# Kernel tuning notes

Hardware: AMD Instinct MI355X
Metric: run time of the kernel (lower is better)

The kernel has to match this reference:

```python
import jax, jax.numpy as jnp
import numpy as np

FEATURE = 256
HIDDEN = 256

def setup_inputs() -> dict:
    key = jax.random.key(0)
    k1, k2, k3 = jax.random.split(key, 3)
    x = jax.random.normal(k1, (64, 2048, FEATURE), dtype=jnp.float32)
    # xavier_normal with gain=0.1: std = 0.1 * sqrt(2/(fan_in+fan_out))
    std_x = 0.1 * np.sqrt(2.0 / (FEATURE + 4 * HIDDEN))
    std_h = 0.1 * np.sqrt(2.0 / (HIDDEN + 4 * HIDDEN))
    WeightX = jax.random.normal(k2, (FEATURE, 4 * HIDDEN), dtype=jnp.float32) * std_x
    WeightH = jax.random.normal(k3, (HIDDEN, 4 * HIDDEN), dtype=jnp.float32) * std_h
    BiasX = jnp.zeros((4 * HIDDEN,), dtype=jnp.float32)
    BiasH = jnp.zeros((4 * HIDDEN,), dtype=jnp.float32)
    return {"x": x, "WeightX": WeightX, "WeightH": WeightH, "BiasX": BiasX, "BiasH": BiasH}

def reference(x, WeightX, WeightH, BiasX, BiasH):
    bs, T, _ = x.shape
    H = WeightH.shape[0]
    # precompute input projection for all timesteps: (bs, T, 4H)
    x_proj = jnp.einsum('btf,fg->btg', x, WeightX) + BiasX + BiasH

    def step(carry, xp_t):
        h, c = carry
        gates = xp_t + h @ WeightH  # (bs, 4H)
        i = jax.nn.sigmoid(gates[:, :H])
        f = jax.nn.sigmoid(gates[:, H:2 * H])
        g = jnp.tanh(gates[:, 2 * H:3 * H])
        o = jax.nn.sigmoid(gates[:, 3 * H:])
        c = f * c + i * g
        h = o * jnp.tanh(c)
        return (h, c), h

    h0 = jnp.zeros((bs, H), dtype=x.dtype)
    c0 = jnp.zeros((bs, H), dtype=x.dtype)
    (h_n, _), out_t = jax.lax.scan(step, (h0, c0), jnp.swapaxes(x_proj, 0, 1))
    output = jnp.swapaxes(out_t, 0, 1)  # (bs, T, H)
    return output, h_n
```

## Files before the change

### kernel.cpp

```cpp
#include <hip/hip_runtime.h>
#include <hip/hip_fp16.h>

#define BATCH 64
#define TSEQ  2048
#define FEAT  256
#define HID   256
#define G4    1024

typedef _Float16 half2_t __attribute__((ext_vector_type(2)));

__device__ __forceinline__ float dot2acc_u(unsigned int a, unsigned int b, float acc) {
    half2_t ah = __builtin_bit_cast(half2_t, a);
    half2_t bh = __builtin_bit_cast(half2_t, b);
#if __has_builtin(__builtin_amdgcn_fdot2)
    return __builtin_amdgcn_fdot2(ah, bh, acc, false);
#else
    return acc + (float)ah.x * (float)bh.x + (float)ah.y * (float)bh.y;
#endif
}

__device__ __forceinline__ float sig_f(float x)  { return 1.f / (1.f + __expf(-x)); }
__device__ __forceinline__ float tanh_f(float x) { return 1.f - 2.f / (__expf(2.f * x) + 1.f); }

__device__ __forceinline__ unsigned int pack2(float a, float b) {
    half2_t h = { (_Float16)a, (_Float16)b };
    return __builtin_bit_cast(unsigned int, h);
}

template <int CTRL>
__device__ __forceinline__ float dpp_add(float x) {
    int y = __builtin_amdgcn_update_dpp(0, __builtin_bit_cast(int, x), CTRL, 0xf, 0xf, true);
    return x + __builtin_bit_cast(float, y);
}

__global__ void wt_convert(const float* __restrict__ WH, uint4* __restrict__ WS,
                           uint4* __restrict__ WST) {
    int idx = blockIdx.x * 256 + threadIdx.x;
    int u = idx >> 13;
    int r = idx & 8191;
    int p = r >> 9;
    int tid = r & 511;
    int w = tid >> 6, c = (tid >> 3) & 7, s = tid & 7;
    int j = p * 64 + w * 8 + c;
    int k0 = 32 * s + 8 * u;
    uint4 v;
    v.x = pack2(WH[(k0 + 0) * G4 + j], WH[(k0 + 1) * G4 + j]);
    v.y = pack2(WH[(k0 + 2) * G4 + j], WH[(k0 + 3) * G4 + j]);
    v.z = pack2(WH[(k0 + 4) * G4 + j], WH[(k0 + 5) * G4 + j]);
    v.w = pack2(WH[(k0 + 6) * G4 + j], WH[(k0 + 7) * G4 + j]);
    if (p < 13) {
        WS[u * 8192 + p * 512 + tid] = v;
    } else {
        int q = p - 13;
        WST[(q * 4 + u) * 512 + tid] = v;
        WST[6144 + (q * 4 + u) * 512 + tid] = v;
    }
}

__global__ __launch_bounds__(256) void xproj_gemm(
    const float* __restrict__ X, const float* __restrict__ WX,
    const float* __restrict__ BX, const float* __restrict__ BH,
    _Float16* __restrict__ XP)
{
    __shared__ float As[64][17];
    __shared__ float Bs[16][68];

    const int tid = threadIdx.x;
    const int tx = tid & 15;
    const int ty = tid >> 4;
    const int rowBase = blockIdx.y * 64;
    const int colBase = blockIdx.x * 64;

    const int ea = tid * 4;
    const int ar = ea >> 4, ac = ea & 15;
    const int br = ea >> 6, bc = ea & 63;

    float acc[4][4] = {};

    for (int kt = 0; kt < FEAT; kt += 16) {
        float4 av = *(const float4*)(X  + (size_t)(rowBase + ar) * FEAT + kt + ac);
        float4 bv = *(const float4*)(WX + (size_t)(kt + br) * G4 + colBase + bc);
        As[ar][ac + 0] = av.x; As[ar][ac + 1] = av.y;
        As[ar][ac + 2] = av.z; As[ar][ac + 3] = av.w;
        *(float4*)&Bs[br][bc] = bv;
        __syncthreads();
        #pragma unroll
        for (int kk = 0; kk < 16; ++kk) {
            float4 b = *(const float4*)&Bs[kk][tx * 4];
            float a0 = As[ty * 4 + 0][kk];
            float a1 = As[ty * 4 + 1][kk];
            float a2 = As[ty * 4 + 2][kk];
            float a3 = As[ty * 4 + 3][kk];
            acc[0][0] = fmaf(a0, b.x, acc[0][0]); acc[0][1] = fmaf(a0, b.y, acc[0][1]);
            acc[0][2] = fmaf(a0, b.z, acc[0][2]); acc[0][3] = fmaf(a0, b.w, acc[0][3]);
            acc[1][0] = fmaf(a1, b.x, acc[1][0]); acc[1][1] = fmaf(a1, b.y, acc[1][1]);
            acc[1][2] = fmaf(a1, b.z, acc[1][2]); acc[1][3] = fmaf(a1, b.w, acc[1][3]);
            acc[2][0] = fmaf(a2, b.x, acc[2][0]); acc[2][1] = fmaf(a2, b.y, acc[2][1]);
            acc[2][2] = fmaf(a2, b.z, acc[2][2]); acc[2][3] = fmaf(a2, b.w, acc[2][3]);
            acc[3][0] = fmaf(a3, b.x, acc[3][0]); acc[3][1] = fmaf(a3, b.y, acc[3][1]);
            acc[3][2] = fmaf(a3, b.z, acc[3][2]); acc[3][3] = fmaf(a3, b.w, acc[3][3]);
        }
        __syncthreads();
    }

    const int n0 = colBase + tx * 4;
    float4 bxv = *(const float4*)(BX + n0);
    float4 bhv = *(const float4*)(BH + n0);
    float bb0 = bxv.x + bhv.x, bb1 = bxv.y + bhv.y;
    float bb2 = bxv.z + bhv.z, bb3 = bxv.w + bhv.w;

    #pragma unroll
    for (int i = 0; i < 4; ++i) {
        int row = rowBase + ty * 4 + i;
        _Float16* p = XP + (size_t)row * G4 + n0;
        half2_t p01 = { (_Float16)(acc[i][0] + bb0), (_Float16)(acc[i][1] + bb1) };
        half2_t p23 = { (_Float16)(acc[i][2] + bb2), (_Float16)(acc[i][3] + bb3) };
        *(half2_t*)(p + 0) = p01;
        *(half2_t*)(p + 2) = p23;
    }
}

#define DO_PASS(P, W0, W1, W2, W3)                                              \
    {                                                                           \
        float acc = 0.f;                                                        \
        acc = dot2acc_u(hr0.x, (W0).x, acc); acc = dot2acc_u(hr0.y, (W0).y, acc); \
        acc = dot2acc_u(hr0.z, (W0).z, acc); acc = dot2acc_u(hr0.w, (W0).w, acc); \
        acc = dot2acc_u(hr1.x, (W1).x, acc); acc = dot2acc_u(hr1.y, (W1).y, acc); \
        acc = dot2acc_u(hr1.z, (W1).z, acc); acc = dot2acc_u(hr1.w, (W1).w, acc); \
        acc = dot2acc_u(hr2.x, (W2).x, acc); acc = dot2acc_u(hr2.y, (W2).y, acc); \
        acc = dot2acc_u(hr2.z, (W2).z, acc); acc = dot2acc_u(hr2.w, (W2).w, acc); \
        acc = dot2acc_u(hr3.x, (W3).x, acc); acc = dot2acc_u(hr3.y, (W3).y, acc); \
        acc = dot2acc_u(hr3.z, (W3).z, acc); acc = dot2acc_u(hr3.w, (W3).w, acc); \
        acc = dpp_add<0xB1>(acc);                                               \
        acc = dpp_add<0x4E>(acc);                                               \
        acc = dpp_add<0x141>(acc);                                              \
        if (s == 0) g_sh[(P) * 64 + w * 8 + c] = acc;                           \
    }

__global__ __launch_bounds__(512, 2) void lstm_rec(
    const _Float16* __restrict__ XP, const uint4* __restrict__ WS,
    const uint4* __restrict__ WST, float* __restrict__ OUT)
{
    __shared__ uint4 LDS_W[4 * 512];
    __shared__ float g_sh[G4];
    __shared__ __align__(16) unsigned short hs[4][64];

    const int tid = threadIdx.x;
    const int b = blockIdx.x;
    const int w = tid >> 6;
    const int c = (tid >> 3) & 7;
    const int s = tid & 7;

    uint4 wreg[48];
    #pragma unroll
    for (int p = 0; p < 12; ++p) {
        #pragma unroll
        for (int u = 0; u < 4; ++u)
            wreg[p * 4 + u] = WS[u * 8192 + p * 512 + tid];
    }
    #pragma unroll
    for (int u = 0; u < 4; ++u)
        LDS_W[u * 512 + tid] = WS[u * 8192 + 12 * 512 + tid];

    if (tid < 256) ((unsigned short*)hs)[tid] = 0;
    float cst = 0.f, hlast = 0.f;
    const _Float16* xpb = XP + (size_t)b * TSEQ * G4;
    float* outb = OUT + (size_t)b * TSEQ * HID;
    __syncthreads();

    #pragma unroll 1
    for (int t = 0; t < TSEQ; ++t) {
        uint4 hr0 = ((const uint4*)(&hs[0][0]))[s];
        uint4 hr1 = ((const uint4*)(&hs[1][0]))[s];
        uint4 hr2 = ((const uint4*)(&hs[2][0]))[s];
        uint4 hr3 = ((const uint4*)(&hs[3][0]))[s];

        float xv0 = 0.f, xv1 = 0.f, xv2 = 0.f, xv3 = 0.f;
        if (tid < 256) {
            const _Float16* xq = xpb + (size_t)t * G4;
            xv0 = (float)xq[tid];       xv1 = (float)xq[tid + 256];
            xv2 = (float)xq[tid + 512]; xv3 = (float)xq[tid + 768];
        }

        const uint4* stb = WST + (size_t)(t & 1) * 6144;
        uint4 pf0 = stb[(0 * 4 + 0) * 512 + tid];
        uint4 pf1 = stb[(0 * 4 + 1) * 512 + tid];
        uint4 pf2 = stb[(0 * 4 + 2) * 512 + tid];
        uint4 pf3 = stb[(0 * 4 + 3) * 512 + tid];

        DO_PASS(0,  wreg[0],  wreg[1],  wreg[2],  wreg[3]);
        DO_PASS(1,  wreg[4],  wreg[5],  wreg[6],  wreg[7]);
        DO_PASS(2,  wreg[8],  wreg[9],  wreg[10], wreg[11]);
        DO_PASS(3,  wreg[12], wreg[13], wreg[14], wreg[15]);
        DO_PASS(4,  wreg[16], wreg[17], wreg[18], wreg[19]);
        DO_PASS(5,  wreg[20], wreg[21], wreg[22], wreg[23]);

        DO_PASS(13, pf0, pf1, pf2, pf3);
        pf0 = stb[(1 * 4 + 0) * 512 + tid];
        pf1 = stb[(1 * 4 + 1) * 512 + tid];
        pf2 = stb[(1 * 4 + 2) * 512 + tid];
        pf3 = stb[(1 * 4 + 3) * 512 + tid];

        DO_PASS(6,  wreg[24], wreg[25], wreg[26], wreg[27]);
        DO_PASS(7,  wreg[28], wreg[29], wreg[30], wreg[31]);
        DO_PASS(8,  wreg[32], wreg[33], wreg[34], wreg[35]);
        DO_PASS(9,  wreg[36], wreg[37], wreg[38], wreg[39]);
        DO_PASS(10, wreg[40], wreg[41], wreg[42], wreg[43]);
        DO_PASS(11, wreg[44], wreg[45], wreg[46], wreg[47]);

        DO_PASS(14, pf0, pf1, pf2, pf3);
        pf0 = stb[(2 * 4 + 0) * 512 + tid];
        pf1 = stb[(2 * 4 + 1) * 512 + tid];
        pf2 = stb[(2 * 4 + 2) * 512 + tid];
        pf3 = stb[(2 * 4 + 3) * 512 + tid];

        {
            uint4 l0 = LDS_W[0 * 512 + tid];
            uint4 l1 = LDS_W[1 * 512 + tid];
            uint4 l2 = LDS_W[2 * 512 + tid];
            uint4 l3 = LDS_W[3 * 512 + tid];
            DO_PASS(12, l0, l1, l2, l3);
        }
        DO_PASS(15, pf0, pf1, pf2, pf3);

        __syncthreads();

        if (tid < 256) {
            float gi = sig_f(g_sh[tid] + xv0);
            float gf = sig_f(g_sh[tid + 256] + xv1);
            float gg = tanh_f(g_sh[tid + 512] + xv2);
            float go = sig_f(g_sh[tid + 768] + xv3);
            cst = gf * cst + gi * gg;
            float h = go * tanh_f(cst);
            outb[(size_t)t * HID + tid] = h;
            hlast = h;
            hs[(tid >> 3) & 3][(tid >> 5) * 8 + (tid & 7)] =
                __builtin_bit_cast(unsigned short, (_Float16)h);
        }
        __syncthreads();
    }

    if (tid < 256)
        OUT[(size_t)BATCH * TSEQ * HID + (size_t)b * HID + tid] = hlast;
}

extern "C" void kernel_launch(void* const* d_in, const int* in_sizes, int n_in,
                              void* d_out, int out_size, void* d_ws, size_t ws_size,
                              hipStream_t stream) {
    const float* x  = (const float*)d_in[0];
    const float* wx = (const float*)d_in[1];
    const float* wh = (const float*)d_in[2];
    const float* bx = (const float*)d_in[3];
    const float* bh = (const float*)d_in[4];
    float* out = (float*)d_out;

    _Float16* xp = (_Float16*)d_ws;
    uint4* ws = (uint4*)((char*)d_ws + (size_t)BATCH * TSEQ * G4 * sizeof(_Float16));
    uint4* wst = ws + 32768;

    hipLaunchKernelGGL(wt_convert, dim3(128), dim3(256), 0, stream, wh, ws, wst);
    hipLaunchKernelGGL(xproj_gemm, dim3(G4 / 64, (BATCH * TSEQ) / 64), dim3(256), 0, stream,
                       x, wx, bx, bh, xp);
    hipLaunchKernelGGL(lstm_rec, dim3(BATCH), dim3(512), 0, stream, xp, ws, wst, out);
}
```

Baseline: 5.674 ms.

## Rebalance recurrent weight residency across registers, LDS and streamed global, prefetch next x-projection

Changes how the recurrent weight matrix is split. Nine gate passes now stay in registers (down from twelve), three sit in LDS (up from one), and four are streamed from global each step (up from three); the duplicated double-buffer copy of the streamed weights is dropped. The next timestep's x-projection load is issued in the middle of the current step so its latency is hidden, and each dot product uses two accumulators to shorten the dependency chain. The aim is to cut register pressure and spills and to overlap load latency on the serial recurrence, at the cost of more LDS and global traffic per step.

```diff
diff --git a/kernel.cpp b/kernel.cpp
--- a/kernel.cpp
+++ b/kernel.cpp
@@ -48,12 +48,11 @@
     v.y = pack2(WH[(k0 + 2) * G4 + j], WH[(k0 + 3) * G4 + j]);
     v.z = pack2(WH[(k0 + 4) * G4 + j], WH[(k0 + 5) * G4 + j]);
     v.w = pack2(WH[(k0 + 6) * G4 + j], WH[(k0 + 7) * G4 + j]);
-    if (p < 13) {
+    if (p < 12) {
         WS[u * 8192 + p * 512 + tid] = v;
     } else {
-        int q = p - 13;
+        int q = p - 12;
         WST[(q * 4 + u) * 512 + tid] = v;
-        WST[6144 + (q * 4 + u) * 512 + tid] = v;
     }
 }
 
@@ -122,26 +121,36 @@
 
 #define DO_PASS(P, W0, W1, W2, W3)                                              \
     {                                                                           \
-        float acc = 0.f;                                                        \
-        acc = dot2acc_u(hr0.x, (W0).x, acc); acc = dot2acc_u(hr0.y, (W0).y, acc); \
-        acc = dot2acc_u(hr0.z, (W0).z, acc); acc = dot2acc_u(hr0.w, (W0).w, acc); \
-        acc = dot2acc_u(hr1.x, (W1).x, acc); acc = dot2acc_u(hr1.y, (W1).y, acc); \
-        acc = dot2acc_u(hr1.z, (W1).z, acc); acc = dot2acc_u(hr1.w, (W1).w, acc); \
-        acc = dot2acc_u(hr2.x, (W2).x, acc); acc = dot2acc_u(hr2.y, (W2).y, acc); \
-        acc = dot2acc_u(hr2.z, (W2).z, acc); acc = dot2acc_u(hr2.w, (W2).w, acc); \
-        acc = dot2acc_u(hr3.x, (W3).x, acc); acc = dot2acc_u(hr3.y, (W3).y, acc); \
-        acc = dot2acc_u(hr3.z, (W3).z, acc); acc = dot2acc_u(hr3.w, (W3).w, acc); \
+        float a0_ = 0.f, a1_ = 0.f;                                             \
+        a0_ = dot2acc_u(hr0.x, (W0).x, a0_); a0_ = dot2acc_u(hr0.y, (W0).y, a0_); \
+        a0_ = dot2acc_u(hr0.z, (W0).z, a0_); a0_ = dot2acc_u(hr0.w, (W0).w, a0_); \
+        a1_ = dot2acc_u(hr1.x, (W1).x, a1_); a1_ = dot2acc_u(hr1.y, (W1).y, a1_); \
+        a1_ = dot2acc_u(hr1.z, (W1).z, a1_); a1_ = dot2acc_u(hr1.w, (W1).w, a1_); \
+        a0_ = dot2acc_u(hr2.x, (W2).x, a0_); a0_ = dot2acc_u(hr2.y, (W2).y, a0_); \
+        a0_ = dot2acc_u(hr2.z, (W2).z, a0_); a0_ = dot2acc_u(hr2.w, (W2).w, a0_); \
+        a1_ = dot2acc_u(hr3.x, (W3).x, a1_); a1_ = dot2acc_u(hr3.y, (W3).y, a1_); \
+        a1_ = dot2acc_u(hr3.z, (W3).z, a1_); a1_ = dot2acc_u(hr3.w, (W3).w, a1_); \
+        float acc = a0_ + a1_;                                                  \
         acc = dpp_add<0xB1>(acc);                                               \
         acc = dpp_add<0x4E>(acc);                                               \
         acc = dpp_add<0x141>(acc);                                              \
         if (s == 0) g_sh[(P) * 64 + w * 8 + c] = acc;                           \
     }
 
+#define LDS_PASS(PP)                                                            \
+    {                                                                           \
+        uint4 l0 = LDS_W[((PP) * 4 + 0) * 512 + tid];                           \
+        uint4 l1 = LDS_W[((PP) * 4 + 1) * 512 + tid];                           \
+        uint4 l2 = LDS_W[((PP) * 4 + 2) * 512 + tid];                           \
+        uint4 l3 = LDS_W[((PP) * 4 + 3) * 512 + tid];                           \
+        DO_PASS(9 + (PP), l0, l1, l2, l3);                                      \
+    }
+
 __global__ __launch_bounds__(512, 2) void lstm_rec(
     const _Float16* __restrict__ XP, const uint4* __restrict__ WS,
     const uint4* __restrict__ WST, float* __restrict__ OUT)
 {
-    __shared__ uint4 LDS_W[4 * 512];
+    __shared__ uint4 LDS_W[3 * 4 * 512];
     __shared__ float g_sh[G4];
     __shared__ __align__(16) unsigned short hs[4][64];
 
@@ -151,21 +160,35 @@
     const int c = (tid >> 3) & 7;
     const int s = tid & 7;
 
-    uint4 wreg[48];
-    #pragma unroll
-    for (int p = 0; p < 12; ++p) {
+    uint4 wreg[36];
+    #pragma unroll
+    for (int p = 0; p < 9; ++p) {
         #pragma unroll
         for (int u = 0; u < 4; ++u)
             wreg[p * 4 + u] = WS[u * 8192 + p * 512 + tid];
     }
     #pragma unroll
-    for (int u = 0; u < 4; ++u)
-        LDS_W[u * 512 + tid] = WS[u * 8192 + 12 * 512 + tid];
+    for (int i = 0; i < 36; ++i)
+        asm volatile("" : "+v"(wreg[i].x), "+v"(wreg[i].y),
+                          "+v"(wreg[i].z), "+v"(wreg[i].w));
+
+    #pragma unroll
+    for (int pp = 0; pp < 3; ++pp) {
+        #pragma unroll
+        for (int u = 0; u < 4; ++u)
+            LDS_W[(pp * 4 + u) * 512 + tid] = WS[u * 8192 + (9 + pp) * 512 + tid];
+    }
 
     if (tid < 256) ((unsigned short*)hs)[tid] = 0;
     float cst = 0.f, hlast = 0.f;
     const _Float16* xpb = XP + (size_t)b * TSEQ * G4;
     float* outb = OUT + (size_t)b * TSEQ * HID;
+
+    float xv0 = 0.f, xv1 = 0.f, xv2 = 0.f, xv3 = 0.f;
+    if (tid < 256) {
+        xv0 = (float)xpb[tid];       xv1 = (float)xpb[tid + 256];
+        xv2 = (float)xpb[tid + 512]; xv3 = (float)xpb[tid + 768];
+    }
     __syncthreads();
 
     #pragma unroll 1
@@ -175,52 +198,58 @@
         uint4 hr2 = ((const uint4*)(&hs[2][0]))[s];
         uint4 hr3 = ((const uint4*)(&hs[3][0]))[s];
 
-        float xv0 = 0.f, xv1 = 0.f, xv2 = 0.f, xv3 = 0.f;
-        if (tid < 256) {
-            const _Float16* xq = xpb + (size_t)t * G4;
-            xv0 = (float)xq[tid];       xv1 = (float)xq[tid + 256];
-            xv2 = (float)xq[tid + 512]; xv3 = (float)xq[tid + 768];
-        }
-
-        const uint4* stb = WST + (size_t)(t & 1) * 6144;
+        uintptr_t stb_i = (uintptr_t)WST;
+        asm volatile("" : "+s"(stb_i));
+        const uint4* stb = (const uint4*)stb_i;
+
         uint4 pf0 = stb[(0 * 4 + 0) * 512 + tid];
         uint4 pf1 = stb[(0 * 4 + 1) * 512 + tid];
         uint4 pf2 = stb[(0 * 4 + 2) * 512 + tid];
         uint4 pf3 = stb[(0 * 4 + 3) * 512 + tid];
 
-        DO_PASS(0,  wreg[0],  wreg[1],  wreg[2],  wreg[3]);
-        DO_PASS(1,  wreg[4],  wreg[5],  wreg[6],  wreg[7]);
-        DO_PASS(2,  wreg[8],  wreg[9],  wreg[10], wreg[11]);
-        DO_PASS(3,  wreg[12], wreg[13], wreg[14], wreg[15]);
-        DO_PASS(4,  wreg[16], wreg[17], wreg[18], wreg[19]);
-        DO_PASS(5,  wreg[20], wreg[21], wreg[22], wreg[23]);
-
-        DO_PASS(13, pf0, pf1, pf2, pf3);
+        DO_PASS(0, wreg[0],  wreg[1],  wreg[2],  wreg[3]);
+        DO_PASS(1, wreg[4],  wreg[5],  wreg[6],  wreg[7]);
+        DO_PASS(2, wreg[8],  wreg[9],  wreg[10], wreg[11]);
+        DO_PASS(3, wreg[12], wreg[13], wreg[14], wreg[15]);
+
+        DO_PASS(12, pf0, pf1, pf2, pf3);
         pf0 = stb[(1 * 4 + 0) * 512 + tid];
         pf1 = stb[(1 * 4 + 1) * 512 + tid];
         pf2 = stb[(1 * 4 + 2) * 512 + tid];
         pf3 = stb[(1 * 4 + 3) * 512 + tid];
 
-        DO_PASS(6,  wreg[24], wreg[25], wreg[26], wreg[27]);
-        DO_PASS(7,  wreg[28], wreg[29], wreg[30], wreg[31]);
-        DO_PASS(8,  wreg[32], wreg[33], wreg[34], wreg[35]);
-        DO_PASS(9,  wreg[36], wreg[37], wreg[38], wreg[39]);
-        DO_PASS(10, wreg[40], wreg[41], wreg[42], wreg[43]);
-        DO_PASS(11, wreg[44], wreg[45], wreg[46], wreg[47]);
-
-        DO_PASS(14, pf0, pf1, pf2, pf3);
+        DO_PASS(4, wreg[16], wreg[17], wreg[18], wreg[19]);
+        DO_PASS(5, wreg[20], wreg[21], wreg[22], wreg[23]);
+        DO_PASS(6, wreg[24], wreg[25], wreg[26], wreg[27]);
+
+        DO_PASS(13, pf0, pf1, pf2, pf3);
         pf0 = stb[(2 * 4 + 0) * 512 + tid];
         pf1 = stb[(2 * 4 + 1) * 512 + tid];
         pf2 = stb[(2 * 4 + 2) * 512 + tid];
         pf3 = stb[(2 * 4 + 3) * 512 + tid];
 
+        DO_PASS(7, wreg[28], wreg[29], wreg[30], wreg[31]);
+        DO_PASS(8, wreg[32], wreg[33], wreg[34], wreg[35]);
+        LDS_PASS(0);
+
+        DO_PASS(14, pf0, pf1, pf2, pf3);
+        pf0 = stb[(3 * 4 + 0) * 512 + tid];
+        pf1 = stb[(3 * 4 + 1) * 512 + tid];
+        pf2 = stb[(3 * 4 + 2) * 512 + tid];
+        pf3 = stb[(3 * 4 + 3) * 512 + tid];
+
+        float xn0 = 0.f, xn1 = 0.f, xn2 = 0.f, xn3 = 0.f;
         {
-            uint4 l0 = LDS_W[0 * 512 + tid];
-            uint4 l1 = LDS_W[1 * 512 + tid];
-            uint4 l2 = LDS_W[2 * 512 + tid];
-            uint4 l3 = LDS_W[3 * 512 + tid];
-            DO_PASS(12, l0, l1, l2, l3);
+            int tn = (t + 1 < TSEQ) ? (t + 1) : t;
+            if (tid < 256) {
+                const _Float16* xq = xpb + (size_t)tn * G4;
+                xn0 = (float)xq[tid];       xn1 = (float)xq[tid + 256];
+                xn2 = (float)xq[tid + 512]; xn3 = (float)xq[tid + 768];
+            }
         }
+
+        LDS_PASS(1);
+        LDS_PASS(2);
         DO_PASS(15, pf0, pf1, pf2, pf3);
 
         __syncthreads();
@@ -237,6 +266,7 @@
             hs[(tid >> 3) & 3][(tid >> 5) * 8 + (tid & 7)] =
                 __builtin_bit_cast(unsigned short, (_Float16)h);
         }
+        xv0 = xn0; xv1 = xn1; xv2 = xn2; xv3 = xn3;
         __syncthreads();
     }
 
```

New measurement: 6.410 ms. +13.0%, slower.

## Split each batch's LSTM recurrence across two blocks with global h exchange

Applied to the files above, without the earlier changes.

Each batch row is now handled by a pair of workgroups, each owning half of the hidden units, so the recurrent weights fit entirely in LDS plus AGPRs and no weights are streamed from global memory each step. The partner's half of h is exchanged every timestep through global memory using release/acquire sequence counters and spin-waiting. The local-half dot products are computed before waiting, to overlap with the exchange, and the next step's input projection is prefetched one step ahead. The cost is a cross-workgroup synchronisation on every timestep, which relies on both blocks of a pair being resident at the same time and adds latency on the serial critical path.

```diff
diff --git a/kernel.cpp b/kernel.cpp
--- a/kernel.cpp
+++ b/kernel.cpp
@@ -34,27 +34,24 @@
 }
 
 __global__ void wt_convert(const float* __restrict__ WH, uint4* __restrict__ WS,
-                           uint4* __restrict__ WST) {
+                           unsigned* __restrict__ SEQ) {
+    if (blockIdx.x == 0 && threadIdx.x < 128) SEQ[threadIdx.x * 32] = 0;
     int idx = blockIdx.x * 256 + threadIdx.x;
-    int u = idx >> 13;
-    int r = idx & 8191;
-    int p = r >> 9;
-    int tid = r & 511;
+    int tid = idx & 511;
+    int u = (idx >> 9) & 3;
+    int pass = (idx >> 11) & 7;
+    int parity = (idx >> 14) & 1;
     int w = tid >> 6, c = (tid >> 3) & 7, s = tid & 7;
-    int j = p * 64 + w * 8 + c;
-    int k0 = 32 * s + 8 * u;
+    int jl = pass * 64 + w * 8 + c;
+    int j = (jl >> 7) * 256 + parity * 128 + (jl & 127);
+    int half_base = ((u < 2) ? parity : 1 - parity) * 128;
+    int k0 = half_base + 16 * s + 8 * (u & 1);
     uint4 v;
     v.x = pack2(WH[(k0 + 0) * G4 + j], WH[(k0 + 1) * G4 + j]);
     v.y = pack2(WH[(k0 + 2) * G4 + j], WH[(k0 + 3) * G4 + j]);
     v.z = pack2(WH[(k0 + 4) * G4 + j], WH[(k0 + 5) * G4 + j]);
     v.w = pack2(WH[(k0 + 6) * G4 + j], WH[(k0 + 7) * G4 + j]);
-    if (p < 13) {
-        WS[u * 8192 + p * 512 + tid] = v;
-    } else {
-        int q = p - 13;
-        WST[(q * 4 + u) * 512 + tid] = v;
-        WST[6144 + (q * 4 + u) * 512 + tid] = v;
-    }
+    WS[((parity * 8 + pass) * 4 + u) * 512 + tid] = v;
 }
 
 __global__ __launch_bounds__(256) void xproj_gemm(
@@ -120,128 +117,192 @@
     }
 }
 
-#define DO_PASS(P, W0, W1, W2, W3)                                              \
+#define DOT8(ACC, H0, H1, W0, W1)                                               \
+    ACC = dot2acc_u((H0).x, (W0).x, ACC); ACC = dot2acc_u((H0).y, (W0).y, ACC); \
+    ACC = dot2acc_u((H0).z, (W0).z, ACC); ACC = dot2acc_u((H0).w, (W0).w, ACC); \
+    ACC = dot2acc_u((H1).x, (W1).x, ACC); ACC = dot2acc_u((H1).y, (W1).y, ACC); \
+    ACC = dot2acc_u((H1).z, (W1).z, ACC); ACC = dot2acc_u((H1).w, (W1).w, ACC);
+
+#define AG_RD(d, a_) asm("v_accvgpr_read_b32 %0, %1" : "=v"(d) : "a"(a_), "s"(t))
+
+#define AG_DOT8(ACC, H0, H1, I0, I1)                                            \
     {                                                                           \
-        float acc = 0.f;                                                        \
-        acc = dot2acc_u(hr0.x, (W0).x, acc); acc = dot2acc_u(hr0.y, (W0).y, acc); \
-        acc = dot2acc_u(hr0.z, (W0).z, acc); acc = dot2acc_u(hr0.w, (W0).w, acc); \
-        acc = dot2acc_u(hr1.x, (W1).x, acc); acc = dot2acc_u(hr1.y, (W1).y, acc); \
-        acc = dot2acc_u(hr1.z, (W1).z, acc); acc = dot2acc_u(hr1.w, (W1).w, acc); \
-        acc = dot2acc_u(hr2.x, (W2).x, acc); acc = dot2acc_u(hr2.y, (W2).y, acc); \
-        acc = dot2acc_u(hr2.z, (W2).z, acc); acc = dot2acc_u(hr2.w, (W2).w, acc); \
-        acc = dot2acc_u(hr3.x, (W3).x, acc); acc = dot2acc_u(hr3.y, (W3).y, acc); \
-        acc = dot2acc_u(hr3.z, (W3).z, acc); acc = dot2acc_u(hr3.w, (W3).w, acc); \
-        acc = dpp_add<0xB1>(acc);                                               \
-        acc = dpp_add<0x4E>(acc);                                               \
-        acc = dpp_add<0x141>(acc);                                              \
-        if (s == 0) g_sh[(P) * 64 + w * 8 + c] = acc;                           \
+        unsigned q0, q1, q2, q3, q4, q5, q6, q7;                                \
+        AG_RD(q0, wa[I0].x); AG_RD(q1, wa[I0].y);                               \
+        AG_RD(q2, wa[I0].z); AG_RD(q3, wa[I0].w);                               \
+        AG_RD(q4, wa[I1].x); AG_RD(q5, wa[I1].y);                               \
+        AG_RD(q6, wa[I1].z); AG_RD(q7, wa[I1].w);                               \
+        ACC = dot2acc_u((H0).x, q0, ACC); ACC = dot2acc_u((H0).y, q1, ACC);     \
+        ACC = dot2acc_u((H0).z, q2, ACC); ACC = dot2acc_u((H0).w, q3, ACC);     \
+        ACC = dot2acc_u((H1).x, q4, ACC); ACC = dot2acc_u((H1).y, q5, ACC);     \
+        ACC = dot2acc_u((H1).z, q6, ACC); ACC = dot2acc_u((H1).w, q7, ACC);     \
     }
 
 __global__ __launch_bounds__(512, 2) void lstm_rec(
     const _Float16* __restrict__ XP, const uint4* __restrict__ WS,
-    const uint4* __restrict__ WST, float* __restrict__ OUT)
+    unsigned* __restrict__ EXD, unsigned* __restrict__ SEQ,
+    float* __restrict__ OUT)
 {
-    __shared__ uint4 LDS_W[4 * 512];
-    __shared__ float g_sh[G4];
-    __shared__ __align__(16) unsigned short hs[4][64];
+    __shared__ uint4 LDS_W[4 * 4 * 512];
+    __shared__ float g_sh[512];
+    __shared__ __align__(16) unsigned short hs[256];
 
     const int tid = threadIdx.x;
-    const int b = blockIdx.x;
+    const int parity = blockIdx.x & 1;
+    const int pair = blockIdx.x >> 1;
     const int w = tid >> 6;
     const int c = (tid >> 3) & 7;
     const int s = tid & 7;
 
-    uint4 wreg[48];
+    unsigned* seq_self = SEQ + (pair * 2 + parity) * 32;
+    unsigned* seq_par  = SEQ + (pair * 2 + (1 - parity)) * 32;
+    unsigned* exd_self = EXD + (pair * 2 + parity) * 2 * 64;
+    unsigned* exd_par  = EXD + (pair * 2 + (1 - parity)) * 2 * 64;
+
+    uint4 wa[16];
     #pragma unroll
-    for (int p = 0; p < 12; ++p) {
+    for (int p = 0; p < 4; ++p) {
+        #pragma unroll
+        for (int u = 0; u < 4; ++u) {
+            uint4 v = WS[((parity * 8 + (4 + p)) * 4 + u) * 512 + tid];
+            asm("v_accvgpr_write_b32 %0, %1" : "=a"(wa[p * 4 + u].x) : "v"(v.x));
+            asm("v_accvgpr_write_b32 %0, %1" : "=a"(wa[p * 4 + u].y) : "v"(v.y));
+            asm("v_accvgpr_write_b32 %0, %1" : "=a"(wa[p * 4 + u].z) : "v"(v.z));
+            asm("v_accvgpr_write_b32 %0, %1" : "=a"(wa[p * 4 + u].w) : "v"(v.w));
+        }
+    }
+    #pragma unroll
+    for (int p = 0; p < 4; ++p) {
         #pragma unroll
         for (int u = 0; u < 4; ++u)
-            wreg[p * 4 + u] = WS[u * 8192 + p * 512 + tid];
-    }
-    #pragma unroll
-    for (int u = 0; u < 4; ++u)
-        LDS_W[u * 512 + tid] = WS[u * 8192 + 12 * 512 + tid];
-
-    if (tid < 256) ((unsigned short*)hs)[tid] = 0;
-    float cst = 0.f, hlast = 0.f;
-    const _Float16* xpb = XP + (size_t)b * TSEQ * G4;
-    float* outb = OUT + (size_t)b * TSEQ * HID;
+            LDS_W[(p * 4 + u) * 512 + tid] = WS[((parity * 8 + p) * 4 + u) * 512 + tid];
+    }
+
+    if (tid < 128) ((unsigned*)hs)[tid] = 0;
+
+    const int pbase = parity * 128;
+    const _Float16* xpb = XP + (size_t)pair * TSEQ * G4;
+    float* outb = OUT + (size_t)pair * TSEQ * HID;
+
+    float c0 = 0.f, c1 = 0.f, hl0 = 0.f, hl1 = 0.f;
+    unsigned xv0 = 0, xv1 = 0, xv2 = 0, xv3 = 0;
+    if (tid < 64) {
+        const _Float16* xq = xpb;
+        xv0 = *(const unsigned*)(xq + 0 * 256 + pbase + 2 * tid);
+        xv1 = *(const unsigned*)(xq + 1 * 256 + pbase + 2 * tid);
+        xv2 = *(const unsigned*)(xq + 2 * 256 + pbase + 2 * tid);
+        xv3 = *(const unsigned*)(xq + 3 * 256 + pbase + 2 * tid);
+    }
     __syncthreads();
 
     #pragma unroll 1
     for (int t = 0; t < TSEQ; ++t) {
-        uint4 hr0 = ((const uint4*)(&hs[0][0]))[s];
-        uint4 hr1 = ((const uint4*)(&hs[1][0]))[s];
-        uint4 hr2 = ((const uint4*)(&hs[2][0]))[s];
-        uint4 hr3 = ((const uint4*)(&hs[3][0]))[s];
-
-        float xv0 = 0.f, xv1 = 0.f, xv2 = 0.f, xv3 = 0.f;
-        if (tid < 256) {
-            const _Float16* xq = xpb + (size_t)t * G4;
-            xv0 = (float)xq[tid];       xv1 = (float)xq[tid + 256];
-            xv2 = (float)xq[tid + 512]; xv3 = (float)xq[tid + 768];
-        }
-
-        const uint4* stb = WST + (size_t)(t & 1) * 6144;
-        uint4 pf0 = stb[(0 * 4 + 0) * 512 + tid];
-        uint4 pf1 = stb[(0 * 4 + 1) * 512 + tid];
-        uint4 pf2 = stb[(0 * 4 + 2) * 512 + tid];
-        uint4 pf3 = stb[(0 * 4 + 3) * 512 + tid];
-
-        DO_PASS(0,  wreg[0],  wreg[1],  wreg[2],  wreg[3]);
-        DO_PASS(1,  wreg[4],  wreg[5],  wreg[6],  wreg[7]);
-        DO_PASS(2,  wreg[8],  wreg[9],  wreg[10], wreg[11]);
-        DO_PASS(3,  wreg[12], wreg[13], wreg[14], wreg[15]);
-        DO_PASS(4,  wreg[16], wreg[17], wreg[18], wreg[19]);
-        DO_PASS(5,  wreg[20], wreg[21], wreg[22], wreg[23]);
-
-        DO_PASS(13, pf0, pf1, pf2, pf3);
-        pf0 = stb[(1 * 4 + 0) * 512 + tid];
-        pf1 = stb[(1 * 4 + 1) * 512 + tid];
-        pf2 = stb[(1 * 4 + 2) * 512 + tid];
-        pf3 = stb[(1 * 4 + 3) * 512 + tid];
-
-        DO_PASS(6,  wreg[24], wreg[25], wreg[26], wreg[27]);
-        DO_PASS(7,  wreg[28], wreg[29], wreg[30], wreg[31]);
-        DO_PASS(8,  wreg[32], wreg[33], wreg[34], wreg[35]);
-        DO_PASS(9,  wreg[36], wreg[37], wreg[38], wreg[39]);
-        DO_PASS(10, wreg[40], wreg[41], wreg[42], wreg[43]);
-        DO_PASS(11, wreg[44], wreg[45], wreg[46], wreg[47]);
-
-        DO_PASS(14, pf0, pf1, pf2, pf3);
-        pf0 = stb[(2 * 4 + 0) * 512 + tid];
-        pf1 = stb[(2 * 4 + 1) * 512 + tid];
-        pf2 = stb[(2 * 4 + 2) * 512 + tid];
-        pf3 = stb[(2 * 4 + 3) * 512 + tid];
-
-        {
-            uint4 l0 = LDS_W[0 * 512 + tid];
-            uint4 l1 = LDS_W[1 * 512 + tid];
-            uint4 l2 = LDS_W[2 * 512 + tid];
-            uint4 l3 = LDS_W[3 * 512 + tid];
-            DO_PASS(12, l0, l1, l2, l3);
-        }
-        DO_PASS(15, pf0, pf1, pf2, pf3);
-
-        __syncthreads();
-
-        if (tid < 256) {
-            float gi = sig_f(g_sh[tid] + xv0);
-            float gf = sig_f(g_sh[tid + 256] + xv1);
-            float gg = tanh_f(g_sh[tid + 512] + xv2);
-            float go = sig_f(g_sh[tid + 768] + xv3);
-            cst = gf * cst + gi * gg;
-            float h = go * tanh_f(cst);
-            outb[(size_t)t * HID + tid] = h;
-            hlast = h;
-            hs[(tid >> 3) & 3][(tid >> 5) * 8 + (tid & 7)] =
-                __builtin_bit_cast(unsigned short, (_Float16)h);
-        }
-        __syncthreads();
-    }
-
-    if (tid < 256)
-        OUT[(size_t)BATCH * TSEQ * HID + (size_t)b * HID + tid] = hlast;
+        const uint4* hso = (const uint4*)((const char*)hs + parity * 256 + 32 * s);
+        uint4 hro0 = hso[0];
+        uint4 hro1 = hso[1];
+
+        unsigned xn0 = 0, xn1 = 0, xn2 = 0, xn3 = 0;
+        if (tid < 64) {
+            int tn = (t + 1 < TSEQ) ? (t + 1) : t;
+            const _Float16* xq = xpb + (size_t)tn * G4;
+            xn0 = *(const unsigned*)(xq + 0 * 256 + pbase + 2 * tid);
+            xn1 = *(const unsigned*)(xq + 1 * 256 + pbase + 2 * tid);
+            xn2 = *(const unsigned*)(xq + 2 * 256 + pbase + 2 * tid);
+            xn3 = *(const unsigned*)(xq + 3 * 256 + pbase + 2 * tid);
+        }
+
+        float pacc[8];
+        #pragma unroll
+        for (int p = 0; p < 4; ++p) {
+            uint4 l0 = LDS_W[(p * 4 + 0) * 512 + tid];
+            uint4 l1 = LDS_W[(p * 4 + 1) * 512 + tid];
+            float a = 0.f;
+            DOT8(a, hro0, hro1, l0, l1);
+            pacc[p] = a;
+        }
+        #pragma unroll
+        for (int p = 0; p < 4; ++p) {
+            float a = 0.f;
+            AG_DOT8(a, hro0, hro1, p * 4 + 0, p * 4 + 1);
+            pacc[4 + p] = a;
+        }
+
+        if (tid < 64 && t > 0) {
+            while (__hip_atomic_load(seq_par, __ATOMIC_ACQUIRE,
+                                     __HIP_MEMORY_SCOPE_AGENT) < (unsigned)t)
+                __builtin_amdgcn_s_sleep(1);
+            unsigned v = __hip_atomic_load(&exd_par[((t - 1) & 1) * 64 + tid],
+                                           __ATOMIC_RELAXED, __HIP_MEMORY_SCOPE_AGENT);
+            ((unsigned*)hs)[(1 - parity) * 64 + tid] = v;
+        }
+        __syncthreads();
+
+        const uint4* hsp = (const uint4*)((const char*)hs + (1 - parity) * 256 + 32 * s);
+        uint4 hrp0 = hsp[0];
+        uint4 hrp1 = hsp[1];
+        #pragma unroll
+        for (int p = 0; p < 4; ++p) {
+            uint4 l2 = LDS_W[(p * 4 + 2) * 512 + tid];
+            uint4 l3 = LDS_W[(p * 4 + 3) * 512 + tid];
+            float a = pacc[p];
+            DOT8(a, hrp0, hrp1, l2, l3);
+            pacc[p] = a;
+        }
+        #pragma unroll
+        for (int p = 0; p < 4; ++p) {
+            float a = pacc[4 + p];
+            AG_DOT8(a, hrp0, hrp1, p * 4 + 2, p * 4 + 3);
+            pacc[4 + p] = a;
+        }
+
+        #pragma unroll
+        for (int p = 0; p < 8; ++p) {
+            float a = pacc[p];
+            a = dpp_add<0xB1>(a);
+            a = dpp_add<0x4E>(a);
+            a = dpp_add<0x141>(a);
+            if (s == 0) g_sh[p * 64 + w * 8 + c] = a;
+        }
+        __syncthreads();
+
+        if (tid < 64) {
+            int e = tid;
+            float2 gi = *(float2*)&g_sh[0 * 128 + 2 * e];
+            float2 gf = *(float2*)&g_sh[1 * 128 + 2 * e];
+            float2 gg = *(float2*)&g_sh[2 * 128 + 2 * e];
+            float2 go = *(float2*)&g_sh[3 * 128 + 2 * e];
+            half2_t xi = __builtin_bit_cast(half2_t, xv0);
+            half2_t xf = __builtin_bit_cast(half2_t, xv1);
+            half2_t xg = __builtin_bit_cast(half2_t, xv2);
+            half2_t xo = __builtin_bit_cast(half2_t, xv3);
+            float i0 = sig_f(gi.x + (float)xi.x),  i1 = sig_f(gi.y + (float)xi.y);
+            float f0 = sig_f(gf.x + (float)xf.x),  f1 = sig_f(gf.y + (float)xf.y);
+            float g0 = tanh_f(gg.x + (float)xg.x), g1 = tanh_f(gg.y + (float)xg.y);
+            float o0 = sig_f(go.x + (float)xo.x),  o1 = sig_f(go.y + (float)xo.y);
+            c0 = f0 * c0 + i0 * g0;
+            c1 = f1 * c1 + i1 * g1;
+            float h0 = o0 * tanh_f(c0);
+            float h1 = o1 * tanh_f(c1);
+            unsigned hp = pack2(h0, h1);
+            __hip_atomic_store(&exd_self[(t & 1) * 64 + e], hp,
+                               __ATOMIC_RELAXED, __HIP_MEMORY_SCOPE_AGENT);
+            if (e == 0)
+                __hip_atomic_store(seq_self, (unsigned)(t + 1),
+                                   __ATOMIC_RELEASE, __HIP_MEMORY_SCOPE_AGENT);
+            ((unsigned*)hs)[parity * 64 + e] = hp;
+            float2 hv; hv.x = h0; hv.y = h1;
+            *(float2*)(outb + (size_t)t * HID + pbase + 2 * e) = hv;
+            hl0 = h0; hl1 = h1;
+        }
+        xv0 = xn0; xv1 = xn1; xv2 = xn2; xv3 = xn3;
+        __syncthreads();
+    }
+
+    if (tid < 64) {
+        float2 hv; hv.x = hl0; hv.y = hl1;
+        *(float2*)(OUT + (size_t)BATCH * TSEQ * HID + (size_t)pair * HID
+                   + pbase + 2 * tid) = hv;
+    }
 }
 
 extern "C" void kernel_launch(void* const* d_in, const int* in_sizes, int n_in,
@@ -256,10 +317,11 @@
 
     _Float16* xp = (_Float16*)d_ws;
     uint4* ws = (uint4*)((char*)d_ws + (size_t)BATCH * TSEQ * G4 * sizeof(_Float16));
-    uint4* wst = ws + 32768;
-
-    hipLaunchKernelGGL(wt_convert, dim3(128), dim3(256), 0, stream, wh, ws, wst);
+    unsigned* exd = (unsigned*)(ws + 32768);
+    unsigned* seq = exd + 16384;
+
+    hipLaunchKernelGGL(wt_convert, dim3(128), dim3(256), 0, stream, wh, ws, seq);
     hipLaunchKernelGGL(xproj_gemm, dim3(G4 / 64, (BATCH * TSEQ) / 64), dim3(256), 0, stream,
                        x, wx, bx, bh, xp);
-    hipLaunchKernelGGL(lstm_rec, dim3(BATCH), dim3(512), 0, stream, xp, ws, wst, out);
-}
+    hipLaunchKernelGGL(lstm_rec, dim3(2 * BATCH), dim3(512), 0, stream, xp, ws, exd, seq, out);
+}
```

Measured after the change: 8.702 ms. 53.4% more time.
